# Optimization experiments

Measured on AMD Instinct MI355X. Metric: run time of the kernel, lower is better.

The kernel has to match this reference:

```python
import jax, jax.numpy as jnp
import numpy as np

G, N, E, F, D = 4096, 64, 256, 64, 128
H1, H2 = 16, 2
EP = 32768
EPS = 1e-15
MAX_LOGSTD = 10.0


def setup_inputs() -> dict:
    key = jax.random.key(0)
    ks = jax.random.split(key, 16)
    def lin(k, i, o):
        return (jax.random.normal(k, (i, o), jnp.float32) / np.sqrt(i)).astype(jnp.float32)
    inp = {}
    inp["x"] = jax.random.normal(ks[0], (G, N, F), jnp.float32)
    inp["edge_index"] = jax.random.randint(ks[1], (G, 2, E), 0, N, dtype=jnp.int32)
    inp["edge_weight"] = jax.random.uniform(ks[2], (G, E), jnp.float32)
    inp["pos_edges"] = jax.random.randint(ks[3], (2, EP), 0, G, dtype=jnp.int32)
    inp["neg_edges"] = jax.random.randint(ks[4], (2, EP), 0, G, dtype=jnp.int32)
    inp["eps"] = jax.random.normal(ks[5], (G, D), jnp.float32)
    inp["W_gcn1"] = lin(ks[6], F, D); inp["b_gcn1"] = jnp.zeros((D,), jnp.float32)
    inp["W_fc1"] = lin(ks[7], D, H1); inp["b_fc1"] = jnp.zeros((H1,), jnp.float32)
    inp["W_fc2"] = lin(ks[8], H1, H2); inp["b_fc2"] = jnp.zeros((H2,), jnp.float32)
    inp["W_c1"] = lin(ks[9], D, 2 * D); inp["b_c1"] = jnp.zeros((2 * D,), jnp.float32)
    inp["W_mu"] = lin(ks[10], 2 * D, D); inp["b_mu"] = jnp.zeros((D,), jnp.float32)
    inp["W_ls"] = lin(ks[11], 2 * D, D); inp["b_ls"] = jnp.zeros((D,), jnp.float32)
    inp["emb"] = jax.random.normal(ks[12], (G, D), jnp.float32)
    inp["W_lin1"] = lin(ks[13], 2 * D, 2 * D); inp["b_lin1"] = jnp.zeros((2 * D,), jnp.float32)
    inp["W_lin2"] = lin(ks[14], 2 * D, 2 * D); inp["b_lin2"] = jnp.zeros((2 * D,), jnp.float32)
    return inp


def gcn_conv(x, src, dst, w, W, b, n):
    # PyG GCNConv: add self-loops (weight 1), sym-normalize, aggregate at target (col).
    xw = x @ W                                      # [n, out]
    deg = jnp.zeros((n,), xw.dtype).at[dst].add(w) + 1.0
    dinv = jax.lax.rsqrt(deg)
    norm = dinv[src] * w * dinv[dst]
    agg = jnp.zeros_like(xw).at[dst].add(xw[src] * norm[:, None])
    agg = agg + xw * (dinv * dinv)[:, None]         # self-loop term
    return agg + b


def sage_graph(x, ei, w, W_gcn1, b_gcn1, W_fc1, b_fc1, W_fc2, b_fc2):
    src, dst = ei[0], ei[1]
    h = gcn_conv(x, src, dst, w, W_gcn1, b_gcn1, N)          # [N, D]
    a1 = jnp.tanh(h @ W_fc1 + b_fc1)                         # [N, H1]
    S = jax.nn.softmax(a1 @ W_fc2 + b_fc2, axis=1)           # [N, 2]
    # get_laplacian(normalization='sym'): L = I - D^{-1/2} A D^{-1/2}, deg from row
    deg = jnp.zeros((N,), x.dtype).at[src].add(w)
    dinv = jnp.where(deg > 0, jax.lax.rsqrt(jnp.maximum(deg, 1e-30)), 0.0)
    lw = -dinv[src] * w * dinv[dst]
    L = jnp.zeros((N, N), x.dtype).at[src, dst].add(lw) + jnp.eye(N, dtype=x.dtype)
    new_adj = S.T @ (L @ S)                                  # [2, 2]
    norm_adj = new_adj / jnp.maximum(jnp.sum(jnp.abs(new_adj), axis=1, keepdims=True), 1e-12)
    diag = jnp.diagonal(norm_adj)
    pos_penalty = jnp.mean((diag - 1.0) ** 2)                # MSE vs ones(2)
    g_emb = jnp.mean(S.T @ h, axis=0)                        # [D]
    return g_emb, pos_penalty


def gcn_conv_unw(x, src, dst, W, b, n):
    return gcn_conv(x, src, dst, jnp.ones(src.shape, x.dtype), W, b, n)


def reference(x, edge_index, edge_weight, pos_edges, neg_edges, eps,
              W_gcn1, b_gcn1, W_fc1, b_fc1, W_fc2, b_fc2,
              W_c1, b_c1, W_mu, b_mu, W_ls, b_ls, emb,
              W_lin1, b_lin1, W_lin2, b_lin2):
    g_embs, pens = jax.vmap(sage_graph,
                            in_axes=(0, 0, 0, None, None, None, None, None, None))(
        x, edge_index, edge_weight, W_gcn1, b_gcn1, W_fc1, b_fc1, W_fc2, b_fc2)
    positive_penalty = jnp.mean(pens)
    # VGAE encode over graph-level graph (dropout in eval mode = identity)
    ps, pd = pos_edges[0], pos_edges[1]
    h = jax.nn.relu(gcn_conv_unw(g_embs, ps, pd, W_c1, b_c1, G))
    mu = gcn_conv_unw(h, ps, pd, W_mu, b_mu, G)
    logstd = jnp.minimum(gcn_conv_unw(h, ps, pd, W_ls, b_ls, G), MAX_LOGSTD)
    z = mu + eps * jnp.exp(logstd)                            # reparametrize
    zc = jnp.concatenate([emb, z], axis=-1)                   # [G, 2D]
    def pred(ei):
        fx = zc[ei[0]] @ W_lin1 + b_lin1
        fy = zc[ei[1]] @ W_lin2 + b_lin2
        return jax.nn.sigmoid(jnp.sum(fx * fy, axis=1))
    pos_pred = pred(pos_edges)
    neg_pred = pred(neg_edges)
    rec_loss = -jnp.mean(jnp.log(pos_pred + EPS)) - jnp.mean(jnp.log(1.0 - neg_pred + EPS))
    kl = -0.5 * jnp.mean(jnp.sum(1.0 + 2.0 * logstd - mu ** 2 - jnp.exp(2.0 * logstd), axis=1))
    pre_loss = rec_loss + kl / G
    return pre_loss, positive_penalty, pos_pred, neg_pred
```

## Files before the change

### kernel.cpp

```cpp
#include <hip/hip_runtime.h>
#include <hip/hip_bf16.h>
#include <math.h>

#define GG   4096
#define NNODE 64
#define EEDGE 256
#define FFEAT 64
#define DDIM 128
#define EP   32768

__device__ __forceinline__ float fast_tanh(float x) {
    float e = __expf(2.0f * x);
    return 1.0f - 2.0f / (e + 1.0f);
}

__global__ void k_prep(const float* __restrict__ Wg, const float* __restrict__ Wf1,
                       const float* __restrict__ bf1, const float* __restrict__ bg,
                       float* __restrict__ Wgf1, float* __restrict__ bcomb,
                       float* __restrict__ bg32, int* __restrict__ icnt_g) {
    int t = threadIdx.x;
    for (int o = t; o < 1024; o += 256) {
        int f = o >> 4, j = o & 15;
        float s = 0.f;
        for (int d = 0; d < 128; ++d) s += Wg[f * 128 + d] * Wf1[d * 16 + j];
        Wgf1[o] = s;
    }
    if (t < 16) {
        float s = bf1[t];
        for (int d = 0; d < 128; ++d) s += bg[d] * Wf1[d * 16 + t];
        bcomb[t] = s;
    }
    if (t >= 128) bg32[t - 128] = 32.0f * bg[t - 128];
    for (int i = t; i < 4096; i += 256) icnt_g[i] = 0;
}

__global__ __launch_bounds__(256) void k_y(
    const float* __restrict__ x, const float* __restrict__ W,
    float* __restrict__ Y)
{
    const int t = threadIdx.x;
    const int rr = t >> 4, jq = (t >> 2) & 3, q = t & 3;
    float4 w[16];
#pragma unroll
    for (int kk = 0; kk < 16; ++kk)
        w[kk] = *(const float4*)&W[(q * 16 + kk) * 16 + jq * 4];
    const size_t rbase = (size_t)blockIdx.x * 256;
#pragma unroll 2
    for (int it = 0; it < 16; ++it) {
        const int n = it * 16 + rr;
        const float* xr = &x[(rbase + n) * 64 + q * 16];
        float xv[16];
        *(float4*)&xv[0]  = *(const float4*)&xr[0];
        *(float4*)&xv[4]  = *(const float4*)&xr[4];
        *(float4*)&xv[8]  = *(const float4*)&xr[8];
        *(float4*)&xv[12] = *(const float4*)&xr[12];
        float4 acc = {0.f, 0.f, 0.f, 0.f};
#pragma unroll
        for (int kk = 0; kk < 16; ++kk) {
            float a = xv[kk];
            acc.x += a * w[kk].x; acc.y += a * w[kk].y;
            acc.z += a * w[kk].z; acc.w += a * w[kk].w;
        }
        acc.x += __shfl_xor(acc.x, 1); acc.x += __shfl_xor(acc.x, 2);
        acc.y += __shfl_xor(acc.y, 1); acc.y += __shfl_xor(acc.y, 2);
        acc.z += __shfl_xor(acc.z, 1); acc.z += __shfl_xor(acc.z, 2);
        acc.w += __shfl_xor(acc.w, 1); acc.w += __shfl_xor(acc.w, 2);
        if (q == 0)
            *(float4*)&Y[(rbase + n) * 16 + jq * 4] = acc;
    }
}

__global__ __launch_bounds__(256) void k_pg(
    const float* __restrict__ Yg, const int* __restrict__ ei, const float* __restrict__ ew,
    const float* __restrict__ x, const float* __restrict__ bcomb,
    const float* __restrict__ Wf2, const float* __restrict__ bf2,
    float* __restrict__ Qh, float* __restrict__ pens)
{
    __shared__ __align__(16) float sm[2624];
    float* Ys    = sm;
    int*   lsrc  = (int*)(sm + 1280);
    float* lnrm  = sm + 1536;
    int*   icnt  = (int*)(sm + 1792);
    int*   offs  = (int*)(sm + 1856);
    int*   curs  = (int*)(sm + 1920);
    float* degw  = sm + 1984;
    float* dinvs = sm + 2048;
    float* deg2s = sm + 2112;
    float* dinv2s= sm + 2176;
    float* cws   = sm + 2240;
    float* Ss    = sm + 2304;
    float* LSs   = sm + 2432;
    float* bcs   = sm + 2560;
    float* Wf2s  = sm + 2576;
    float* bf2s  = sm + 2608;

    const int g = blockIdx.x;
    const int t = threadIdx.x;
    const int n = t >> 2, q = t & 3;

    int es, ed; float wv;
    {
        const int* eg = ei + (size_t)g * 512;
        es = eg[t];
        ed = eg[256 + t];
        wv = ew[(size_t)g * 256 + t];
        *(float4*)&Ys[n * 20 + q * 4] = *(const float4*)&Yg[(size_t)g * 1024 + t * 4];
        if (t < 16) bcs[t] = bcomb[t];
        if (t < 32) Wf2s[t] = Wf2[t];
        if (t < 2)  bf2s[t] = bf2[t];
        if (t < 64) { icnt[t] = 0; degw[t] = 1.0f; deg2s[t] = 0.0f; }
        if (t < 128) LSs[t] = 0.0f;
    }
    __syncthreads();

    atomicAdd(&icnt[ed], 1);
    atomicAdd(&degw[ed], wv);
    atomicAdd(&deg2s[es], wv);
    __syncthreads();

    if (t < 64) {
        int v = icnt[t], own = v;
        for (int o = 1; o < 64; o <<= 1) { int u = __shfl_up(v, o); if (t >= o) v += u; }
        int excl = v - own;
        offs[t] = excl; curs[t] = excl;
        float dv = rsqrtf(degw[t]);
        dinvs[t] = dv;
        cws[t] = dv * dv;
        float dg = deg2s[t];
        dinv2s[t] = dg > 0.0f ? rsqrtf(fmaxf(dg, 1e-30f)) : 0.0f;
    }
    __syncthreads();

    float lw;
    {
        int pos = atomicAdd(&curs[ed], 1);
        float nm = dinvs[es] * wv * dinvs[ed];
        lsrc[pos] = es;
        lnrm[pos] = nm;
        atomicAdd(&cws[es], nm);
        lw = -dinv2s[es] * wv * dinv2s[ed];
    }
    __syncthreads();

    {
        float dv = dinvs[n];
        float sc = dv * dv;
        float4 acc = *(const float4*)&Ys[n * 20 + q * 4];
        acc.x *= sc; acc.y *= sc; acc.z *= sc; acc.w *= sc;
        int o = offs[n], c = icnt[n];
        for (int j = 0; j < c; ++j) {
            int s = lsrc[o + j];
            float nm = lnrm[o + j];
            float4 yv = *(const float4*)&Ys[s * 20 + q * 4];
            acc.x += yv.x * nm; acc.y += yv.y * nm;
            acc.z += yv.z * nm; acc.w += yv.w * nm;
        }
        float4 bc4 = *(const float4*)&bcs[q * 4];
        float t0 = fast_tanh(acc.x + bc4.x);
        float t1 = fast_tanh(acc.y + bc4.y);
        float t2 = fast_tanh(acc.z + bc4.z);
        float t3 = fast_tanh(acc.w + bc4.w);
        float4 wf0 = *(const float4*)&Wf2s[8 * q];
        float4 wf1 = *(const float4*)&Wf2s[8 * q + 4];
        float z0 = t0 * wf0.x + t1 * wf0.z + t2 * wf1.x + t3 * wf1.z;
        float z1 = t0 * wf0.y + t1 * wf0.w + t2 * wf1.y + t3 * wf1.w;
        z0 += __shfl_xor(z0, 1); z0 += __shfl_xor(z0, 2);
        z1 += __shfl_xor(z1, 1); z1 += __shfl_xor(z1, 2);
        if (q == 0) {
            z0 += bf2s[0]; z1 += bf2s[1];
            float m = fmaxf(z0, z1);
            float e0 = __expf(z0 - m), e1 = __expf(z1 - m);
            float inv = 1.0f / (e0 + e1);
            Ss[n * 2] = e0 * inv; Ss[n * 2 + 1] = e1 * inv;
        }
    }
    __syncthreads();

    {
        float s0 = Ss[ed * 2], s1 = Ss[ed * 2 + 1];
        atomicAdd(&LSs[es * 2],     lw * s0);
        atomicAdd(&LSs[es * 2 + 1], lw * s1);
    }
    __syncthreads();

    if (t < 64) {
        float s0 = Ss[t * 2], s1 = Ss[t * 2 + 1];
        float l0 = s0 + LSs[t * 2], l1 = s1 + LSs[t * 2 + 1];
        float p00 = s0 * l0, p01 = s0 * l1, p10 = s1 * l0, p11 = s1 * l1;
        for (int o = 32; o; o >>= 1) {
            p00 += __shfl_down(p00, o); p01 += __shfl_down(p01, o);
            p10 += __shfl_down(p10, o); p11 += __shfl_down(p11, o);
        }
        if (t == 0) {
            float r0 = fmaxf(fabsf(p00) + fabsf(p01), 1e-12f);
            float r1 = fmaxf(fabsf(p10) + fabsf(p11), 1e-12f);
            float d0 = p00 / r0 - 1.0f, d1 = p11 / r1 - 1.0f;
            pens[g] = 0.5f * (d0 * d0 + d1 * d1);
        }
    }
    {
        int k = t & 63, p = t >> 6;
        const float* xg = x + (size_t)g * 4096 + k;
        float qk = 0.f;
#pragma unroll 4
        for (int nn = p * 16; nn < p * 16 + 16; ++nn)
            qk += cws[nn] * xg[(size_t)nn * 64];
        __syncthreads();
        Ys[p * 64 + k] = qk;
    }
    __syncthreads();
    if (t < 64)
        Qh[(size_t)g * 64 + t] = 0.5f * (Ys[t] + Ys[64 + t] + Ys[128 + t] + Ys[192 + t]);
}

__global__ void k_cnt(const int* __restrict__ pd, int* __restrict__ icnt) {
    int e = blockIdx.x * 256 + threadIdx.x;
    atomicAdd(&icnt[pd[e]], 1);
}

__global__ void k_scan(const int* __restrict__ icnt, int* __restrict__ offs,
                       int* __restrict__ curs, float* __restrict__ dinv) {
    __shared__ int wsum[4];
    int t = threadIdx.x;
    int base = t * 16;
    int l0,l1,l2,l3,l4,l5,l6,l7,l8,l9,l10,l11,l12,l13,l14,l15;
    l0=icnt[base+0]; l1=icnt[base+1]; l2=icnt[base+2]; l3=icnt[base+3];
    l4=icnt[base+4]; l5=icnt[base+5]; l6=icnt[base+6]; l7=icnt[base+7];
    l8=icnt[base+8]; l9=icnt[base+9]; l10=icnt[base+10]; l11=icnt[base+11];
    l12=icnt[base+12]; l13=icnt[base+13]; l14=icnt[base+14]; l15=icnt[base+15];
    int s = l0+l1+l2+l3+l4+l5+l6+l7+l8+l9+l10+l11+l12+l13+l14+l15;
    int lane = t & 63, w = t >> 6;
    int v = s;
    for (int o = 1; o < 64; o <<= 1) { int u = __shfl_up(v, o); if (lane >= o) v += u; }
    if (lane == 63) wsum[w] = v;
    __syncthreads();
    int woff = 0;
    for (int i = 0; i < 4; ++i) if (i < w) woff += wsum[i];
    int run = woff + v - s;
#define SC(L, I) offs[base+(I)] = run; curs[base+(I)] = run; \
    dinv[base+(I)] = rsqrtf((float)(L) + 1.0f); run += L;
    SC(l0,0) SC(l1,1) SC(l2,2) SC(l3,3) SC(l4,4) SC(l5,5) SC(l6,6) SC(l7,7)
    SC(l8,8) SC(l9,9) SC(l10,10) SC(l11,11) SC(l12,12) SC(l13,13) SC(l14,14) SC(l15,15)
#undef SC
}

__global__ void k_place(const int* __restrict__ pe, const float* __restrict__ dinv,
                        int* __restrict__ curs, int* __restrict__ csr_src,
                        float* __restrict__ csr_nrm) {
    int e = blockIdx.x * 256 + threadIdx.x;
    int s = pe[e], d = pe[EP + e];
    int pos = atomicAdd(&curs[d], 1);
    csr_src[pos] = s;
    csr_nrm[pos] = dinv[s] * dinv[d];
}

__global__ void k_gather128(const int* __restrict__ offs, const int* __restrict__ icnt,
                            const int* __restrict__ csr_src, const float* __restrict__ csr_nrm,
                            const float* __restrict__ dinv, const float* __restrict__ in,
                            float* __restrict__ out) {
    int g = blockIdx.x, d = threadIdx.x;
    float dv = dinv[g];
    float acc = in[(size_t)g * 128 + d] * dv * dv;
    int o = offs[g], c = icnt[g];
    for (int j = 0; j < c; ++j)
        acc += in[(size_t)csr_src[o + j] * 128 + d] * csr_nrm[o + j];
    out[(size_t)g * 128 + d] = acc;
}

__global__ void k_gather256(const int* __restrict__ offs, const int* __restrict__ icnt,
                            const int* __restrict__ csr_src, const float* __restrict__ csr_nrm,
                            const float* __restrict__ dinv, const float* __restrict__ in,
                            float* __restrict__ out) {
    int g = blockIdx.x, d = threadIdx.x;
    float dv = dinv[g];
    float acc = in[(size_t)g * 256 + d] * dv * dv;
    int o = offs[g], c = icnt[g];
    for (int j = 0; j < c; ++j)
        acc += in[(size_t)csr_src[o + j] * 256 + d] * csr_nrm[o + j];
    out[(size_t)g * 256 + d] = acc;
}

__global__ __launch_bounds__(256) void k_gemm(
    const float* __restrict__ A,
    const float* __restrict__ B0, const float* __restrict__ bias0, float* __restrict__ C0,
    const float* __restrict__ B1, const float* __restrict__ bias1, float* __restrict__ C1,
    int M, int K, int N, int dorelu)
{
    __shared__ __align__(16) float lds[2 * 4352];
    const float* B = B0; const float* bias = bias0; float* C = C0;
    int by = blockIdx.y;
    if (B1 != nullptr && by >= (int)(gridDim.y >> 1)) {
        B = B1; bias = bias1; C = C1; by -= (gridDim.y >> 1);
    }
    const int mb = blockIdx.x * 64, nbb = by * 64;
    const int t = threadIdx.x;
    const int tm4 = (t >> 4) * 4, tn4 = (t & 15) * 4;
    const int ma = t >> 2, ka = (t & 3) * 8;
    const int kb = t >> 3, nb8 = (t & 7) * 8;

    float4 pa0, pa1, pb0, pb1;
#define LOADT(K0) { \
    const float* Ap = &A[(size_t)(mb + ma) * K + (K0) + ka]; \
    pa0 = *(const float4*)Ap; pa1 = *(const float4*)(Ap + 4); \
    const float* Bp = &B[(size_t)((K0) + kb) * N + nbb + nb8]; \
    pb0 = *(const float4*)Bp; pb1 = *(const float4*)(Bp + 4); }
#define STORET(BUF) { \
    float* At_ = lds + (BUF) * 4352; \
    At_[(ka + 0) * 68 + ma] = pa0.x; At_[(ka + 1) * 68 + ma] = pa0.y; \
    At_[(ka + 2) * 68 + ma] = pa0.z; At_[(ka + 3) * 68 + ma] = pa0.w; \
    At_[(ka + 4) * 68 + ma] = pa1.x; At_[(ka + 5) * 68 + ma] = pa1.y; \
    At_[(ka + 6) * 68 + ma] = pa1.z; At_[(ka + 7) * 68 + ma] = pa1.w; \
    float* Bs_ = lds + (BUF) * 4352 + 2176; \
    *(float4*)&Bs_[kb * 68 + nb8] = pb0; *(float4*)&Bs_[kb * 68 + nb8 + 4] = pb1; }

    float4 ca0 = {0,0,0,0}, ca1 = {0,0,0,0}, ca2 = {0,0,0,0}, ca3 = {0,0,0,0};
    const int nk0 = K >> 5;
    LOADT(0)
    STORET(0)
    __syncthreads();
    for (int it = 0; it < nk0; ++it) {
        if (it + 1 < nk0) LOADT((it + 1) * 32)
        const float* At_ = lds + (it & 1) * 4352;
        const float* Bs_ = At_ + 2176;
#pragma unroll
        for (int k = 0; k < 32; ++k) {
            float4 av = *(const float4*)&At_[k * 68 + tm4];
            float4 bv = *(const float4*)&Bs_[k * 68 + tn4];
            ca0.x += av.x * bv.x; ca0.y += av.x * bv.y; ca0.z += av.x * bv.z; ca0.w += av.x * bv.w;
            ca1.x += av.y * bv.x; ca1.y += av.y * bv.y; ca1.z += av.y * bv.z; ca1.w += av.y * bv.w;
            ca2.x += av.z * bv.x; ca2.y += av.z * bv.y; ca2.z += av.z * bv.z; ca2.w += av.z * bv.w;
            ca3.x += av.w * bv.x; ca3.y += av.w * bv.y; ca3.z += av.w * bv.z; ca3.w += av.w * bv.w;
        }
        if (it + 1 < nk0) {
            STORET((it + 1) & 1)
            __syncthreads();
        }
    }
#undef LOADT
#undef STORET
    float4 bv4 = {0, 0, 0, 0};
    if (bias) bv4 = *(const float4*)&bias[nbb + tn4];
#define CST(I, CV) { \
    float4 v; v.x = CV.x + bv4.x; v.y = CV.y + bv4.y; v.z = CV.z + bv4.z; v.w = CV.w + bv4.w; \
    if (dorelu) { v.x = fmaxf(v.x, 0.f); v.y = fmaxf(v.y, 0.f); v.z = fmaxf(v.z, 0.f); v.w = fmaxf(v.w, 0.f); } \
    *(float4*)&C[(size_t)(mb + tm4 + (I)) * N + nbb + tn4] = v; }
    CST(0, ca0) CST(1, ca1) CST(2, ca2) CST(3, ca3)
#undef CST
}

__global__ void k_fin_z(const float* __restrict__ mu_arr, const float* __restrict__ ls_arr,
                        const float* __restrict__ eps, const float* __restrict__ emb,
                        float* __restrict__ zc, float* __restrict__ klp) {
    __shared__ float smw[2];
    int g = blockIdx.x, d = threadIdx.x;
    int idx = g * 128 + d;
    float mu = mu_arr[idx];
    float ls = fminf(ls_arr[idx], 10.0f);
    float e  = __expf(ls);
    float z = mu + eps[idx] * e;
    zc[(size_t)g * 256 + d] = emb[idx];
    zc[(size_t)g * 256 + 128 + d] = z;
    float term = 1.0f + 2.0f * ls - mu * mu - e * e;
    for (int o = 32; o; o >>= 1) term += __shfl_down(term, o);
    if ((d & 63) == 0) smw[d >> 6] = term;
    __syncthreads();
    if (d == 0) klp[g] = smw[0] + smw[1];
}

__global__ void k_pred(const float* __restrict__ A, const float* __restrict__ B,
                       const int* __restrict__ pos, const int* __restrict__ neg,
                       float* __restrict__ out, float* __restrict__ predp) {
    __shared__ float smw[16];
    int t = threadIdx.x, sub = t >> 4, l = t & 15;
    int eg = blockIdx.x * 16 + sub;
    int isneg = eg >= EP;
    int e = eg - (isneg ? EP : 0);
    const int* eix = isneg ? neg : pos;
    int s = eix[e], d = eix[EP + e];
    const float4* Ar = (const float4*)(A + (size_t)s * 256);
    const float4* Br = (const float4*)(B + (size_t)d * 256);
    float dot = 0.f;
#pragma unroll
    for (int q = 0; q < 4; ++q) {
        float4 av = Ar[l + 16 * q], bv = Br[l + 16 * q];
        dot += av.x * bv.x + av.y * bv.y + av.z * bv.z + av.w * bv.w;
    }
    for (int o = 8; o; o >>= 1) dot += __shfl_down(dot, o);
    if (l == 0) {
        float p = 1.0f / (1.0f + __expf(-dot));
        float term;
        if (isneg) { out[2 + EP + e] = p; term = __logf(1.0f - p + 1e-15f); }
        else       { out[2 + e] = p;      term = __logf(p + 1e-15f); }
        smw[sub] = term;
    }
    __syncthreads();
    if (t == 0) {
        float s16 = 0.f;
#pragma unroll
        for (int i = 0; i < 16; ++i) s16 += smw[i];
        predp[blockIdx.x] = s16;
    }
}

__global__ void k_final(const float* __restrict__ pens, const float* __restrict__ klp,
                        const float* __restrict__ predp, float* __restrict__ out) {
    __shared__ float sm[16];
    int t = threadIdx.x;
    float s_pen = 0.f, s_kl = 0.f, s_pos = 0.f, s_neg = 0.f;
    for (int i = t; i < 4096; i += 256) { s_pen += pens[i]; s_kl += klp[i]; }
    for (int i = t; i < 2048; i += 256) { s_pos += predp[i]; s_neg += predp[2048 + i]; }
    for (int o = 32; o; o >>= 1) {
        s_pen += __shfl_down(s_pen, o); s_kl += __shfl_down(s_kl, o);
        s_pos += __shfl_down(s_pos, o); s_neg += __shfl_down(s_neg, o);
    }
    int w = t >> 6;
    if ((t & 63) == 0) { sm[w] = s_pen; sm[4 + w] = s_kl; sm[8 + w] = s_pos; sm[12 + w] = s_neg; }
    __syncthreads();
    if (t == 0) {
        float pen = sm[0] + sm[1] + sm[2] + sm[3];
        float kls = sm[4] + sm[5] + sm[6] + sm[7];
        float pos = sm[8] + sm[9] + sm[10] + sm[11];
        float neg = sm[12] + sm[13] + sm[14] + sm[15];
        float rec = -(pos / 32768.0f) - (neg / 32768.0f);
        out[0] = rec - 0.5f * kls / (4096.0f * 4096.0f);
        out[1] = pen * (1.0f / 4096.0f);
    }
}

extern "C" void kernel_launch(void* const* d_in, const int* in_sizes, int n_in,
                              void* d_out, int out_size, void* d_ws, size_t ws_size,
                              hipStream_t stream) {
    const float* x   = (const float*)d_in[0];
    const int*   ei  = (const int*)d_in[1];
    const float* ew  = (const float*)d_in[2];
    const int*   pos = (const int*)d_in[3];
    const int*   neg = (const int*)d_in[4];
    const float* eps = (const float*)d_in[5];
    const float* Wg  = (const float*)d_in[6];
    const float* bg  = (const float*)d_in[7];
    const float* Wf1 = (const float*)d_in[8];
    const float* bf1 = (const float*)d_in[9];
    const float* Wf2 = (const float*)d_in[10];
    const float* bf2 = (const float*)d_in[11];
    const float* Wc1 = (const float*)d_in[12];
    const float* bc1 = (const float*)d_in[13];
    const float* Wmu = (const float*)d_in[14];
    const float* bmu = (const float*)d_in[15];
    const float* Wls = (const float*)d_in[16];
    const float* bls = (const float*)d_in[17];
    const float* emb = (const float*)d_in[18];
    const float* Wl1 = (const float*)d_in[19];
    const float* bl1 = (const float*)d_in[20];
    const float* Wl2 = (const float*)d_in[21];
    const float* bl2 = (const float*)d_in[22];
    float* out = (float*)d_out;
    float* ws  = (float*)d_ws;

    float* g_embs  = ws + 0;
    float* dinv    = ws + 524288;
    int*   icnt_g  = (int*)(ws + 528384);
    int*   off_g   = (int*)(ws + 532480);
    int*   cur_g   = (int*)(ws + 536576);
    int*   csr_src = (int*)(ws + 540672);
    float* csr_nrm = ws + 573440;
    float* Qh      = ws + 606208;
    float* ga      = ws + 868352;
    float* h       = ws + 1392640;
    float* ha      = ws + 2441216;
    float* mu_arr  = ws + 3489792;
    float* ls_arr  = ws + 4014080;
    float* zc      = ws + 4538368;
    float* Abuf    = ws + 5586944;
    float* Bbuf    = ws + 6635520;
    float* pens    = ws + 7684096;
    float* klp     = ws + 7688192;
    float* predp   = ws + 7692288;
    float* Wgf1    = ws + 7708672;
    float* bcomb   = ws + 7709696;
    float* bg32    = ws + 7709712;
    float* Y       = ws + 1392640;

    k_prep<<<1, 256, 0, stream>>>(Wg, Wf1, bf1, bg, Wgf1, bcomb, bg32, icnt_g);
    k_y<<<1024, 256, 0, stream>>>(x, Wgf1, Y);
    k_pg<<<GG, 256, 0, stream>>>(Y, ei, ew, x, bcomb, Wf2, bf2, Qh, pens);
    k_gemm<<<dim3(64, 2), 256, 0, stream>>>(Qh, Wg, bg32, g_embs,
                                            nullptr, nullptr, nullptr, GG, 64, 128, 0);

    k_cnt<<<EP / 256, 256, 0, stream>>>(pos + EP, icnt_g);
    k_scan<<<1, 256, 0, stream>>>(icnt_g, off_g, cur_g, dinv);
    k_place<<<EP / 256, 256, 0, stream>>>(pos, dinv, cur_g, csr_src, csr_nrm);

    k_gather128<<<GG, 128, 0, stream>>>(off_g, icnt_g, csr_src, csr_nrm, dinv, g_embs, ga);
    k_gemm<<<dim3(64, 4), 256, 0, stream>>>(ga, Wc1, bc1, h,
                                            nullptr, nullptr, nullptr, GG, 128, 256, 1);

    k_gather256<<<GG, 256, 0, stream>>>(off_g, icnt_g, csr_src, csr_nrm, dinv, h, ha);
    k_gemm<<<dim3(64, 4), 256, 0, stream>>>(ha, Wmu, bmu, mu_arr,
                                            Wls, bls, ls_arr, GG, 256, 128, 0);
    k_fin_z<<<GG, 128, 0, stream>>>(mu_arr, ls_arr, eps, emb, zc, klp);

    k_gemm<<<dim3(64, 8), 256, 0, stream>>>(zc, Wl1, bl1, Abuf,
                                            Wl2, bl2, Bbuf, GG, 256, 256, 0);

    k_pred<<<(2 * EP) / 16, 256, 0, stream>>>(Abuf, Bbuf, pos, neg, out, predp);
    k_final<<<1, 256, 0, stream>>>(pens, klp, predp, out);
}
```

Baseline: 331.1 us.

## Fold link-predictor weights into single bilinear matrix and bias terms

The two per-node projections zc@W_lin1 and zc@W_lin2 are replaced by one projection U = zc @ (W_lin1 W_lin2^T). The edge score becomes zc[s]·U[d] plus per-node bias terms and a constant, with those terms computed in k_prep and k_fin_z. This halves the dual-output GEMM work, at the cost of an extra small kernel that builds the 256x256 matrix, and changes the floating-point summation order.

New measurement: 344.6 us. 1.04x slower.

```diff
diff --git a/kernel.cpp b/kernel.cpp
--- a/kernel.cpp
+++ b/kernel.cpp
@@ -16,8 +16,13 @@
 
 __global__ void k_prep(const float* __restrict__ Wg, const float* __restrict__ Wf1,
                        const float* __restrict__ bf1, const float* __restrict__ bg,
+                       const float* __restrict__ Wl1, const float* __restrict__ bl1,
+                       const float* __restrict__ Wl2, const float* __restrict__ bl2,
                        float* __restrict__ Wgf1, float* __restrict__ bcomb,
-                       float* __restrict__ bg32, int* __restrict__ icnt_g) {
+                       float* __restrict__ bg32, int* __restrict__ icnt_g,
+                       float* __restrict__ w1b2, float* __restrict__ w2b1,
+                       float* __restrict__ cconst) {
+    __shared__ float cred[4];
     int t = threadIdx.x;
     for (int o = t; o < 1024; o += 256) {
         int f = o >> 4, j = o & 15;
@@ -32,6 +37,38 @@
     }
     if (t >= 128) bg32[t - 128] = 32.0f * bg[t - 128];
     for (int i = t; i < 4096; i += 256) icnt_g[i] = 0;
+    {
+        const float* r1 = Wl1 + (size_t)t * 256;
+        const float* r2 = Wl2 + (size_t)t * 256;
+        float s1 = 0.f, s2 = 0.f;
+        for (int j = 0; j < 256; ++j) { s1 += r1[j] * bl2[j]; s2 += r2[j] * bl1[j]; }
+        w1b2[t] = s1; w2b1[t] = s2;
+    }
+    {
+        float p = bl1[t] * bl2[t];
+        for (int o = 32; o; o >>= 1) p += __shfl_down(p, o);
+        if ((t & 63) == 0) cred[t >> 6] = p;
+        __syncthreads();
+        if (t == 0) cconst[0] = cred[0] + cred[1] + cred[2] + cred[3];
+    }
+}
+
+__global__ __launch_bounds__(256) void k_mt(const float* __restrict__ Wl1,
+                                            const float* __restrict__ Wl2,
+                                            float* __restrict__ MT) {
+    __shared__ __align__(16) float r2[256];
+    const int m = blockIdx.x, k = threadIdx.x;
+    if (k < 64) *(float4*)&r2[k * 4] = *(const float4*)&Wl2[(size_t)m * 256 + k * 4];
+    __syncthreads();
+    const float* r1 = Wl1 + (size_t)k * 256;
+    float acc = 0.f;
+#pragma unroll 8
+    for (int j4 = 0; j4 < 64; ++j4) {
+        float4 a = *(const float4*)&r1[j4 * 4];
+        float4 b = *(const float4*)&r2[j4 * 4];
+        acc += a.x * b.x + a.y * b.y + a.z * b.z + a.w * b.w;
+    }
+    MT[(size_t)m * 256 + k] = acc;
 }
 
 __global__ __launch_bounds__(256) void k_y(
@@ -350,24 +387,39 @@
 
 __global__ void k_fin_z(const float* __restrict__ mu_arr, const float* __restrict__ ls_arr,
                         const float* __restrict__ eps, const float* __restrict__ emb,
-                        float* __restrict__ zc, float* __restrict__ klp) {
-    __shared__ float smw[2];
+                        const float* __restrict__ w1b2, const float* __restrict__ w2b1,
+                        float* __restrict__ zc, float* __restrict__ klp,
+                        float* __restrict__ a_arr, float* __restrict__ b_arr) {
+    __shared__ float smw[6];
     int g = blockIdx.x, d = threadIdx.x;
     int idx = g * 128 + d;
     float mu = mu_arr[idx];
     float ls = fminf(ls_arr[idx], 10.0f);
     float e  = __expf(ls);
     float z = mu + eps[idx] * e;
-    zc[(size_t)g * 256 + d] = emb[idx];
+    float em = emb[idx];
+    zc[(size_t)g * 256 + d] = em;
     zc[(size_t)g * 256 + 128 + d] = z;
     float term = 1.0f + 2.0f * ls - mu * mu - e * e;
-    for (int o = 32; o; o >>= 1) term += __shfl_down(term, o);
-    if ((d & 63) == 0) smw[d >> 6] = term;
-    __syncthreads();
-    if (d == 0) klp[g] = smw[0] + smw[1];
-}
-
-__global__ void k_pred(const float* __restrict__ A, const float* __restrict__ B,
+    float av = em * w1b2[d] + z * w1b2[128 + d];
+    float bv = em * w2b1[d] + z * w2b1[128 + d];
+    for (int o = 32; o; o >>= 1) {
+        term += __shfl_down(term, o);
+        av   += __shfl_down(av, o);
+        bv   += __shfl_down(bv, o);
+    }
+    if ((d & 63) == 0) { int w = d >> 6; smw[w] = term; smw[2 + w] = av; smw[4 + w] = bv; }
+    __syncthreads();
+    if (d == 0) {
+        klp[g]   = smw[0] + smw[1];
+        a_arr[g] = smw[2] + smw[3];
+        b_arr[g] = smw[4] + smw[5];
+    }
+}
+
+__global__ void k_pred(const float* __restrict__ ZC, const float* __restrict__ U,
+                       const float* __restrict__ a_arr, const float* __restrict__ b_arr,
+                       const float* __restrict__ cconst,
                        const int* __restrict__ pos, const int* __restrict__ neg,
                        float* __restrict__ out, float* __restrict__ predp) {
     __shared__ float smw[16];
@@ -377,8 +429,8 @@
     int e = eg - (isneg ? EP : 0);
     const int* eix = isneg ? neg : pos;
     int s = eix[e], d = eix[EP + e];
-    const float4* Ar = (const float4*)(A + (size_t)s * 256);
-    const float4* Br = (const float4*)(B + (size_t)d * 256);
+    const float4* Ar = (const float4*)(ZC + (size_t)s * 256);
+    const float4* Br = (const float4*)(U + (size_t)d * 256);
     float dot = 0.f;
 #pragma unroll
     for (int q = 0; q < 4; ++q) {
@@ -387,6 +439,7 @@
     }
     for (int o = 8; o; o >>= 1) dot += __shfl_down(dot, o);
     if (l == 0) {
+        dot += a_arr[s] + b_arr[d] + cconst[0];
         float p = 1.0f / (1.0f + __expf(-dot));
         float term;
         if (isneg) { out[2 + EP + e] = p; term = __logf(1.0f - p + 1e-15f); }
@@ -470,17 +523,24 @@
     float* mu_arr  = ws + 3489792;
     float* ls_arr  = ws + 4014080;
     float* zc      = ws + 4538368;
-    float* Abuf    = ws + 5586944;
-    float* Bbuf    = ws + 6635520;
+    float* Ubuf    = ws + 5586944;
+    float* MT      = ws + 6635520;
+    float* w1b2    = ws + 6701056;
+    float* w2b1    = ws + 6701312;
+    float* cconst  = ws + 6701568;
     float* pens    = ws + 7684096;
     float* klp     = ws + 7688192;
     float* predp   = ws + 7692288;
+    float* a_arr   = ws + 7696384;
+    float* b_arr   = ws + 7700480;
     float* Wgf1    = ws + 7708672;
     float* bcomb   = ws + 7709696;
     float* bg32    = ws + 7709712;
     float* Y       = ws + 1392640;
 
-    k_prep<<<1, 256, 0, stream>>>(Wg, Wf1, bf1, bg, Wgf1, bcomb, bg32, icnt_g);
+    k_prep<<<1, 256, 0, stream>>>(Wg, Wf1, bf1, bg, Wl1, bl1, Wl2, bl2,
+                                  Wgf1, bcomb, bg32, icnt_g, w1b2, w2b1, cconst);
+    k_mt<<<256, 256, 0, stream>>>(Wl1, Wl2, MT);
     k_y<<<1024, 256, 0, stream>>>(x, Wgf1, Y);
     k_pg<<<GG, 256, 0, stream>>>(Y, ei, ew, x, bcomb, Wf2, bf2, Qh, pens);
     k_gemm<<<dim3(64, 2), 256, 0, stream>>>(Qh, Wg, bg32, g_embs,
@@ -497,11 +557,13 @@
     k_gather256<<<GG, 256, 0, stream>>>(off_g, icnt_g, csr_src, csr_nrm, dinv, h, ha);
     k_gemm<<<dim3(64, 4), 256, 0, stream>>>(ha, Wmu, bmu, mu_arr,
                                             Wls, bls, ls_arr, GG, 256, 128, 0);
-    k_fin_z<<<GG, 128, 0, stream>>>(mu_arr, ls_arr, eps, emb, zc, klp);
-
-    k_gemm<<<dim3(64, 8), 256, 0, stream>>>(zc, Wl1, bl1, Abuf,
-                                            Wl2, bl2, Bbuf, GG, 256, 256, 0);
-
-    k_pred<<<(2 * EP) / 16, 256, 0, stream>>>(Abuf, Bbuf, pos, neg, out, predp);
+    k_fin_z<<<GG, 128, 0, stream>>>(mu_arr, ls_arr, eps, emb, w1b2, w2b1,
+                                    zc, klp, a_arr, b_arr);
+
+    k_gemm<<<dim3(64, 4), 256, 0, stream>>>(zc, MT, nullptr, Ubuf,
+                                            nullptr, nullptr, nullptr, GG, 256, 256, 0);
+
+    k_pred<<<(2 * EP) / 16, 256, 0, stream>>>(zc, Ubuf, a_arr, b_arr, cconst,
+                                              pos, neg, out, predp);
     k_final<<<1, 256, 0, stream>>>(pens, klp, predp, out);
 }
```
